# Performance work log

Hardware: AMD Instinct MI355X
Metric: run time of the kernel (lower is better)

## Reference

```python
import jax, jax.numpy as jnp
import numpy as np

NEG_SLOPE = 0.2  # PyG GATConv default negative_slope
H, C = 4, 64     # heads, per-head channels


def gat_layer(x, src, dst, edge_attr, W, a_src, a_dst, We, a_e, b):
    """PyG-style GATConv with edge features, concat=True. src/dst include self loops."""
    N = x.shape[0]
    h = (x @ W).reshape(N, H, C)                      # [N,H,C]
    al_s = (h * a_src[None]).sum(-1)                  # [N,H]
    al_d = (h * a_dst[None]).sum(-1)                  # [N,H]
    eh = (edge_attr @ We).reshape(-1, H, C)           # [E,H,C]
    al_e = (eh * a_e[None]).sum(-1)                   # [E,H]
    alpha = jax.nn.leaky_relu(al_s[src] + al_d[dst] + al_e, NEG_SLOPE)  # [E,H]
    # softmax over incoming edges of each destination node
    m = jax.ops.segment_max(alpha, dst, num_segments=N)
    p = jnp.exp(alpha - m[dst])
    denom = jax.ops.segment_sum(p, dst, num_segments=N)
    w = p / (denom[dst] + 1e-16)                      # [E,H]
    msg = h[src] * w[..., None]                       # [E,H,C]
    out = jax.ops.segment_sum(msg, dst, num_segments=N)  # [N,H,C]
    return out.reshape(N, H * C) + b


def setup_inputs() -> dict:
    key = jax.random.key(0)
    ks = jax.random.split(key, 20)
    N, E = 50000, 800000
    s = 0.05
    inp = {
        'x': jax.random.normal(ks[0], (N, 5), jnp.float32),
        'edge_index': jax.random.randint(ks[1], (2, E), 0, N, jnp.int32),
        'edge_attr': jax.random.normal(ks[2], (E, 4), jnp.float32),
        'W0': jax.random.normal(ks[3], (5, 256), jnp.float32) * s,
        'a_src0': jax.random.normal(ks[4], (H, C), jnp.float32) * s,
        'a_dst0': jax.random.normal(ks[5], (H, C), jnp.float32) * s,
        'We0': jax.random.normal(ks[6], (4, 256), jnp.float32) * s,
        'a_e0': jax.random.normal(ks[7], (H, C), jnp.float32) * s,
        'b0': jnp.zeros((256,), jnp.float32),
        'W1': jax.random.normal(ks[8], (256, 256), jnp.float32) * s,
        'a_src1': jax.random.normal(ks[9], (H, C), jnp.float32) * s,
        'a_dst1': jax.random.normal(ks[10], (H, C), jnp.float32) * s,
        'We1': jax.random.normal(ks[11], (4, 256), jnp.float32) * s,
        'a_e1': jax.random.normal(ks[12], (H, C), jnp.float32) * s,
        'b1': jnp.zeros((256,), jnp.float32),
        'Wm1': jax.random.normal(ks[13], (768, 128), jnp.float32) * s,
        'bm1': jnp.zeros((128,), jnp.float32),
        'Wm2': jax.random.normal(ks[14], (128, 64), jnp.float32) * s,
        'bm2': jnp.zeros((64,), jnp.float32),
        'Wm3': jax.random.normal(ks[15], (64, 128), jnp.float32) * s,
        'bm3': jnp.zeros((128,), jnp.float32),
    }
    return inp


def reference(x, edge_index, edge_attr,
              W0, a_src0, a_dst0, We0, a_e0, b0,
              W1, a_src1, a_dst1, We1, a_e1, b1,
              Wm1, bm1, Wm2, bm2, Wm3, bm3):
    N = x.shape[0]
    # add self loops once; self-loop edge_attr = mean of edge_attr (PyG fill_value='mean')
    loops = jnp.arange(N, dtype=edge_index.dtype)
    src = jnp.concatenate([edge_index[0], loops])
    dst = jnp.concatenate([edge_index[1], loops])
    mean_ea = jnp.mean(edge_attr, axis=0, keepdims=True)
    ea = jnp.concatenate([edge_attr, jnp.broadcast_to(mean_ea, (N, edge_attr.shape[1]))], axis=0)

    h = gat_layer(x, src, dst, ea, W0, a_src0, a_dst0, We0, a_e0, b0)
    h = jax.nn.relu(h)  # dropout is identity in eval
    h = gat_layer(h, src, dst, ea, W1, a_src1, a_dst1, We1, a_e1, b1)

    mean_pool = jnp.mean(h, axis=0)                      # [256]
    max_pool = jnp.max(h, axis=0)                        # [256]
    att = jax.nn.softmax(jnp.sum(h * mean_pool[None], axis=1))  # [N]
    att_pool = jnp.sum(h * att[:, None], axis=0)         # [256]
    comb = jnp.concatenate([mean_pool, max_pool, att_pool])  # [768]

    z = jax.nn.relu(comb @ Wm1 + bm1)
    z = jax.nn.relu(z @ Wm2 + bm2)
    g = z @ Wm3 + bm3
    return g[None]  # [1,128]
```

## Files before the change

### kernel.cpp

```cpp
#include <hip/hip_runtime.h>
#include <hip/hip_fp16.h>
#include <type_traits>

static const long long N_ = 50000;
static const long long E_ = 800000;
#define LOG2E 1.44269504088896f

typedef __attribute__((ext_vector_type(8))) short bf16x8;
typedef __attribute__((ext_vector_type(4))) float f32x4;

__device__ __forceinline__ float lrelu(float x){ return x >= 0.f ? x : 0.2f*x; }
__device__ __forceinline__ unsigned fkey(float x){
  unsigned u = __float_as_uint(x);
  return (u & 0x80000000u) ? ~u : (u | 0x80000000u);
}
__device__ __forceinline__ float unfkey(unsigned k){
  return __uint_as_float((k & 0x80000000u) ? (k & 0x7fffffffu) : ~k);
}
__device__ __forceinline__ unsigned h2u(__half2 h){ return *(unsigned*)&h; }

__global__ void k_pre(const int* __restrict__ ei, int* __restrict__ deg,
                      const float* __restrict__ ea, float* __restrict__ sum_ea,
                      const float* __restrict__ W1, ushort* __restrict__ Bhi,
                      ushort* __restrict__ Blo){
  int t = threadIdx.x;
  long long e = (long long)blockIdx.x*256 + t;
  if (e < E_) atomicAdd(&deg[ei[E_ + e]], 1);
  if (blockIdx.x < 256){
    int k = blockIdx.x, n = t;
    float v = W1[k*256+n];
    unsigned u = __float_as_uint(v);
    ushort hi = (ushort)(u>>16);
    float rem = v - __uint_as_float(u & 0xffff0000u);
    unsigned ur = __float_as_uint(rem);
    ushort lo = (ushort)((ur + 0x7fff + ((ur>>16)&1)) >> 16);
    int tl = n>>4, kb = k>>5, q = (k>>3)&3, j = k&7;
    long long idx = ((((long long)tl*8+kb)*64 + q*16 + (n&15))<<3) + j;
    Bhi[idx] = hi; Blo[idx] = lo;
  }
  __shared__ float lds[256];
  float s = 0.f;
  for (long long i = (long long)blockIdx.x*256 + t; i < E_*4; i += (long long)gridDim.x*256)
    s += ea[i];
  lds[t] = s; __syncthreads();
  for (int st=128; st>=4; st>>=1){ if (t<st) lds[t] += lds[t+st]; __syncthreads(); }
  if (t<4) atomicAdd(&sum_ea[t], lds[t]);
}

__global__ void k_scan1(const int* __restrict__ deg, int* __restrict__ bsum){
  __shared__ int lds[256];
  int t = threadIdx.x;
  long long idx = (long long)blockIdx.x*256 + t;
  lds[t] = (idx < N_) ? deg[idx] : 0;
  __syncthreads();
  for (int st=128; st>=1; st>>=1){ if (t<st) lds[t] += lds[t+st]; __syncthreads(); }
  if (t==0) bsum[blockIdx.x] = lds[0];
}

__global__ void k_scan2(const int* __restrict__ bsum, int* __restrict__ bpre, int nb,
                        int* __restrict__ rowptr,
                        const float* __restrict__ We0, const float* __restrict__ ae0,
                        const float* __restrict__ We1, const float* __restrict__ ae1,
                        const float* __restrict__ sum_ea, float* __restrict__ small){
  __shared__ int lds[256];
  int t = threadIdx.x;
  int v = (t < nb) ? bsum[t] : 0;
  lds[t] = v; __syncthreads();
  for (int off=1; off<256; off<<=1){
    int add = (t>=off) ? lds[t-off] : 0;
    __syncthreads();
    lds[t] += add;
    __syncthreads();
  }
  if (t < nb) bpre[t] = lds[t] - v;
  if (t == 0) rowptr[N_] = (int)E_;
  if (t < 32){
    int l = t>>4, f = (t>>2)&3, h = t&3;
    const float* We = l ? We1 : We0;
    const float* ae = l ? ae1 : ae0;
    float s = 0.f;
    for (int cc=0; cc<64; cc++) s += We[f*256 + h*64 + cc]*ae[h*64+cc];
    small[l*16 + f*4 + h] = s * LOG2E;
  }
  __syncthreads();
  if (t < 8){
    int l = t>>2, h = t&3;
    const float* Ae = small + l*16;
    const float invE = 1.f/(float)E_;
    float s = 0.f;
    for (int f=0; f<4; f++) s += sum_ea[f]*invE*Ae[f*4+h];
    small[32 + l*4 + h] = s;
  }
}

__global__ void k_scan3(const int* __restrict__ deg, const int* __restrict__ bpre,
                        int* __restrict__ rowptr, int* __restrict__ cursor){
  __shared__ int lds[256];
  int t = threadIdx.x;
  long long idx = (long long)blockIdx.x*256 + t;
  int v = (idx < N_) ? deg[idx] : 0;
  lds[t] = v; __syncthreads();
  for (int off=1; off<256; off<<=1){
    int add = (t>=off) ? lds[t-off] : 0;
    __syncthreads();
    lds[t] += add;
    __syncthreads();
  }
  if (idx < N_){
    int rp = bpre[blockIdx.x] + lds[t] - v;
    rowptr[idx] = rp; cursor[idx] = rp;
  }
}

__global__ void k_scatter(const int* __restrict__ ei, const float* __restrict__ ea,
                          int* __restrict__ cursor, int* __restrict__ csr_src,
                          __half* __restrict__ aleh, const float* __restrict__ small){
  long long e = (long long)blockIdx.x*256 + threadIdx.x;
  if (e >= E_) return;
  int s = ei[e], d = ei[E_+e];
  int pos = atomicAdd(&cursor[d], 1);
  csr_src[pos] = s;
  float4 v = *(const float4*)(ea + e*4);
  float o0[4], o1[4];
  #pragma unroll
  for (int h=0; h<4; h++){
    o0[h] = v.x*small[0+h]  + v.y*small[4+h]  + v.z*small[8+h]  + v.w*small[12+h];
    o1[h] = v.x*small[16+h] + v.y*small[20+h] + v.z*small[24+h] + v.w*small[28+h];
  }
  uint4 pk = make_uint4(h2u(__floats2half2_rn(o0[0],o0[1])),
                        h2u(__floats2half2_rn(o0[2],o0[3])),
                        h2u(__floats2half2_rn(o1[0],o1[1])),
                        h2u(__floats2half2_rn(o1[2],o1[3])));
  *(uint4*)(aleh + (long long)pos*8) = pk;
}

__global__ void k_h0(const float* __restrict__ x, const float* __restrict__ W0,
                     const float* __restrict__ as0, const float* __restrict__ ad0,
                     __half* __restrict__ h0, float* __restrict__ als, float* __restrict__ ald){
  int wid = (int)(((long long)blockIdx.x*blockDim.x + threadIdx.x) >> 6);
  int lane = threadIdx.x & 63;
  if (wid >= (int)N_) return;
  const float* xr = x + wid*5;
  float xv[5];
  #pragma unroll
  for (int f=0; f<5; f++) xv[f] = xr[f];
  int c = lane*4;
  float a0=0,a1=0,a2=0,a3=0;
  #pragma unroll
  for (int f=0; f<5; f++){
    const float* wr = W0 + f*256 + c;
    a0 += xv[f]*wr[0]; a1 += xv[f]*wr[1]; a2 += xv[f]*wr[2]; a3 += xv[f]*wr[3];
  }
  __half2 p01 = __floats2half2_rn(a0,a1);
  __half2 p23 = __floats2half2_rn(a2,a3);
  uint2 pk = make_uint2(h2u(p01), h2u(p23));
  *(uint2*)(h0 + wid*256 + c) = pk;
  const float* asp = as0 + c;
  const float* adp = ad0 + c;
  float ss = a0*asp[0]+a1*asp[1]+a2*asp[2]+a3*asp[3];
  float dd = a0*adp[0]+a1*adp[1]+a2*adp[2]+a3*adp[3];
  int head = lane>>4;
  #pragma unroll
  for (int m=1; m<16; m<<=1){ ss += __shfl_xor(ss, m); dd += __shfl_xor(dd, m); }
  if ((lane&15)==0){ als[wid*4+head]=ss*LOG2E; ald[wid*4+head]=dd*LOG2E; }
}

template<typename OutT, bool RELU>
__global__ __launch_bounds__(256) void k_agg(const __half* __restrict__ hin,
    const float* __restrict__ als, const float* __restrict__ ald,
    const int* __restrict__ rowptr, const int* __restrict__ csr_src,
    const __half* __restrict__ aleh,
    const float* __restrict__ small, int loop_off,
    const float* __restrict__ bias, OutT* __restrict__ out){
  int wid = (int)(((long long)blockIdx.x*256 + threadIdx.x) >> 6);
  int lane = threadIdx.x & 63;
  if (wid >= (int)N_) return;
  int head = lane>>4, c = lane*4;
  const uint2* hp = (const uint2*)hin;
  float aldv = ald[wid*4+head];
  float aS = lrelu(als[wid*4+head] + aldv + small[loop_off+head]);
  float mA = aS, dA = 1.f;
  uint2 pk0 = hp[wid*64 + lane];
  float2 f01 = __half22float2(*(__half2*)&pk0.x);
  float2 f23 = __half22float2(*(__half2*)&pk0.y);
  float aAx=f01.x, aAy=f01.y, aAz=f23.x, aAw=f23.y;
  float mB=-1e30f, dB=0.f, aBx=0.f, aBy=0.f, aBz=0.f, aBw=0.f;
  int beg = rowptr[wid], end = rowptr[wid+1];
  int i = beg;
  for (; i+3 < end; i+=4){
    int s0=csr_src[i], s1=csr_src[i+1], s2=csr_src[i+2], s3=csr_src[i+3];
    float t0=als[s0*4+head], t1=als[s1*4+head];
    float t2=als[s2*4+head], t3=als[s3*4+head];
    float e0=__half2float(aleh[i*8+head]);
    float e1=__half2float(aleh[(i+1)*8+head]);
    float e2=__half2float(aleh[(i+2)*8+head]);
    float e3=__half2float(aleh[(i+3)*8+head]);
    uint2 r0=hp[s0*64+lane], r1=hp[s1*64+lane];
    uint2 r2=hp[s2*64+lane], r3=hp[s3*64+lane];
    float a0=lrelu(t0+aldv+e0), a1=lrelu(t1+aldv+e1);
    float a2=lrelu(t2+aldv+e2), a3=lrelu(t3+aldv+e3);
    {
      float nm = fmaxf(mA, fmaxf(a0,a1));
      float sc = exp2f(mA-nm), p0 = exp2f(a0-nm), p1 = exp2f(a1-nm);
      float2 u01=__half22float2(*(__half2*)&r0.x), u23=__half22float2(*(__half2*)&r0.y);
      float2 v01=__half22float2(*(__half2*)&r1.x), v23=__half22float2(*(__half2*)&r1.y);
      dA  = dA*sc + p0 + p1;
      aAx = aAx*sc + p0*u01.x + p1*v01.x;
      aAy = aAy*sc + p0*u01.y + p1*v01.y;
      aAz = aAz*sc + p0*u23.x + p1*v23.x;
      aAw = aAw*sc + p0*u23.y + p1*v23.y;
      mA = nm;
    }
    {
      float nm = fmaxf(mB, fmaxf(a2,a3));
      float sc = exp2f(mB-nm), p2 = exp2f(a2-nm), p3 = exp2f(a3-nm);
      float2 u01=__half22float2(*(__half2*)&r2.x), u23=__half22float2(*(__half2*)&r2.y);
      float2 v01=__half22float2(*(__half2*)&r3.x), v23=__half22float2(*(__half2*)&r3.y);
      dB  = dB*sc + p2 + p3;
      aBx = aBx*sc + p2*u01.x + p3*v01.x;
      aBy = aBy*sc + p2*u01.y + p3*v01.y;
      aBz = aBz*sc + p2*u23.x + p3*v23.x;
      aBw = aBw*sc + p2*u23.y + p3*v23.y;
      mB = nm;
    }
  }
  for (; i < end; i++){
    int s0 = csr_src[i];
    float e0 = __half2float(aleh[i*8+head]);
    float a = lrelu(als[s0*4+head] + aldv + e0);
    uint2 r = hp[s0*64+lane];
    float nm = fmaxf(mA, a);
    float sc = exp2f(mA-nm), p = exp2f(a-nm);
    float2 g01=__half22float2(*(__half2*)&r.x), g23=__half22float2(*(__half2*)&r.y);
    dA  = dA*sc + p;
    aAx = aAx*sc + p*g01.x;
    aAy = aAy*sc + p*g01.y;
    aAz = aAz*sc + p*g23.x;
    aAw = aAw*sc + p*g23.y;
    mA = nm;
  }
  float nm = fmaxf(mA, mB);
  float sA = exp2f(mA-nm), sB = exp2f(mB-nm);
  float d  = dA*sA + dB*sB;
  float ax = aAx*sA + aBx*sB, ay = aAy*sA + aBy*sB;
  float az = aAz*sA + aBz*sB, aw = aAw*sA + aBw*sB;
  float inv = 1.f/(d + 1e-16f);
  const float* bp = bias + c;
  float ox = ax*inv + bp[0], oy = ay*inv + bp[1];
  float oz = az*inv + bp[2], ow = aw*inv + bp[3];
  if (RELU){ ox=fmaxf(ox,0.f); oy=fmaxf(oy,0.f); oz=fmaxf(oz,0.f); ow=fmaxf(ow,0.f); }
  if constexpr (std::is_same<OutT,__half>::value){
    uint2 qk = make_uint2(h2u(__floats2half2_rn(ox,oy)), h2u(__floats2half2_rn(oz,ow)));
    *(uint2*)(out + wid*256 + c) = qk;
  } else {
    *(float4*)(out + wid*256 + c) = make_float4(ox,oy,oz,ow);
  }
}

__global__ __launch_bounds__(256) void k_gemm(const float* __restrict__ A,
    const ushort* __restrict__ Bhi, const ushort* __restrict__ Blo,
    __half* __restrict__ Ch, const float* __restrict__ as1, const float* __restrict__ ad1,
    float* __restrict__ als, float* __restrict__ ald){
  __shared__ ushort Ah[32*264];
  __shared__ ushort Al[32*264];
  int t = threadIdx.x;
  long long base = (long long)blockIdx.x*32;
  for (int i=t; i<2048; i+=256){
    int r = i>>6, q4 = i&63;
    float4 v = make_float4(0.f,0.f,0.f,0.f);
    if (base + r < N_) v = *(const float4*)(A + (base+r)*256 + q4*4);
    float vv[4] = {v.x,v.y,v.z,v.w};
    ushort hh[4], ll[4];
    #pragma unroll
    for (int e=0;e<4;e++){
      unsigned u = __float_as_uint(vv[e]);
      hh[e] = (ushort)(u>>16);
      float rem = vv[e] - __uint_as_float(u & 0xffff0000u);
      unsigned ur = __float_as_uint(rem);
      ll[e] = (ushort)((ur + 0x7fff + ((ur>>16)&1)) >> 16);
    }
    int off = r*264 + q4*4;
    *(ushort4*)(Ah+off) = make_ushort4(hh[0],hh[1],hh[2],hh[3]);
    *(ushort4*)(Al+off) = make_ushort4(ll[0],ll[1],ll[2],ll[3]);
  }
  __syncthreads();
  int w = t>>6, lane = t&63, m = lane&15, q = lane>>4;
  int rbase = (w>>1)*16;
  int nhalf = (w&1)*8;
  f32x4 acc[8];
  #pragma unroll
  for (int i=0;i<8;i++) acc[i] = (f32x4){0.f,0.f,0.f,0.f};
  for (int kb=0; kb<8; kb++){
    int aoff = (rbase+m)*264 + kb*32 + q*8;
    bf16x8 ah = *(const bf16x8*)(Ah + aoff);
    bf16x8 al = *(const bf16x8*)(Al + aoff);
    #pragma unroll
    for (int tt=0; tt<8; tt++){
      long long bidx = ((((long long)(nhalf+tt)*8+kb)*64 + lane)<<3);
      bf16x8 bh = *(const bf16x8*)(Bhi + bidx);
      bf16x8 bl = *(const bf16x8*)(Blo + bidx);
      acc[tt] = __builtin_amdgcn_mfma_f32_16x16x32_bf16(ah, bh, acc[tt], 0,0,0);
      acc[tt] = __builtin_amdgcn_mfma_f32_16x16x32_bf16(al, bh, acc[tt], 0,0,0);
      acc[tt] = __builtin_amdgcn_mfma_f32_16x16x32_bf16(ah, bl, acc[tt], 0,0,0);
    }
  }
  float ssv[4][2], ddv[4][2];
  #pragma unroll
  for (int r=0;r<4;r++){ ssv[r][0]=0.f; ssv[r][1]=0.f; ddv[r][0]=0.f; ddv[r][1]=0.f; }
  #pragma unroll
  for (int tt=0; tt<8; tt++){
    int col = (nhalf+tt)*16 + m;
    float as_ = as1[col], ad_ = ad1[col];
    int hh = tt>>2;
    #pragma unroll
    for (int r=0;r<4;r++){
      ssv[r][hh] += acc[tt][r]*as_;
      ddv[r][hh] += acc[tt][r]*ad_;
    }
  }
  #pragma unroll
  for (int r=0;r<4;r++){
    #pragma unroll
    for (int hh=0; hh<2; hh++){
      #pragma unroll
      for (int mm=1; mm<16; mm<<=1){
        ssv[r][hh] += __shfl_xor(ssv[r][hh], mm);
        ddv[r][hh] += __shfl_xor(ddv[r][hh], mm);
      }
    }
  }
  #pragma unroll
  for (int r=0;r<4;r++){
    long long grow = base + rbase + q*4 + r;
    if (grow < N_){
      #pragma unroll
      for (int tt=0; tt<8; tt++)
        Ch[grow*256 + (nhalf+tt)*16 + m] = __float2half(acc[tt][r]);
      if (m==0){
        int hb = (w&1)*2;
        als[grow*4 + hb+0] = ssv[r][0]*LOG2E;
        ald[grow*4 + hb+0] = ddv[r][0]*LOG2E;
        als[grow*4 + hb+1] = ssv[r][1]*LOG2E;
        ald[grow*4 + hb+1] = ddv[r][1]*LOG2E;
      }
    }
  }
}

__global__ void k_pool1(const __half* __restrict__ h2, float* __restrict__ sum_pool,
                        unsigned* __restrict__ maxkey){
  int c = threadIdx.x;
  float s = 0.f; float m = -3.4e38f;
  for (long long n = blockIdx.x; n < N_; n += gridDim.x){
    float v = __half2float(h2[n*256+c]); s += v; m = fmaxf(m, v);
  }
  atomicAdd(&sum_pool[c], s);
  atomicMax(&maxkey[c], fkey(m));
}

__global__ void k_atts(const __half* __restrict__ h2, const float* __restrict__ sum_pool,
                       float* __restrict__ sarr, unsigned* __restrict__ smax){
  __shared__ float lmax[4];
  int t = threadIdx.x; int lane = t&63; int w = t>>6;
  const float invN = 1.f/(float)N_;
  int c = lane*4;
  float4 mp = *(const float4*)(sum_pool + c);
  float mymax = -3.4e38f;
  for (long long wid = (long long)blockIdx.x*4 + w; wid < N_; wid += (long long)gridDim.x*4){
    uint2 pk = *(const uint2*)(h2 + wid*256 + c);
    float2 a01 = __half22float2(*(__half2*)&pk.x);
    float2 a23 = __half22float2(*(__half2*)&pk.y);
    float s = (a01.x*mp.x + a01.y*mp.y + a23.x*mp.z + a23.y*mp.w)*invN;
    #pragma unroll
    for (int m=1; m<64; m<<=1) s += __shfl_xor(s, m);
    if (lane==0) sarr[wid] = s;
    mymax = fmaxf(mymax, s);
  }
  if (lane==0) lmax[w] = mymax;
  __syncthreads();
  if (t==0){
    float mm = fmaxf(fmaxf(lmax[0],lmax[1]), fmaxf(lmax[2],lmax[3]));
    atomicMax(smax, fkey(mm));
  }
}

__global__ void k_attd(const float* __restrict__ sarr, const unsigned* __restrict__ smax,
                       float* __restrict__ ssum){
  __shared__ float lds[256];
  int t = threadIdx.x;
  float mx = unfkey(*smax);
  float s = 0.f;
  for (long long i = (long long)blockIdx.x*256 + t; i < N_; i += (long long)gridDim.x*256)
    s += __expf(sarr[i] - mx);
  lds[t] = s; __syncthreads();
  for (int st=128; st>=1; st>>=1){ if (t<st) lds[t]+=lds[t+st]; __syncthreads(); }
  if (t==0) atomicAdd(ssum, lds[0]);
}

__global__ void k_attp(const __half* __restrict__ h2, const float* __restrict__ sarr,
                       const unsigned* __restrict__ smax, const float* __restrict__ ssum,
                       float* __restrict__ att_pool){
  int c = threadIdx.x;
  float mx = unfkey(*smax);
  float inv = 1.f/(*ssum);
  float acc = 0.f;
  for (long long n = blockIdx.x; n < N_; n += gridDim.x){
    float w = __expf(sarr[n]-mx)*inv;
    acc += __half2float(h2[n*256+c])*w;
  }
  atomicAdd(&att_pool[c], acc);
}

__global__ void k_mlp(const float* __restrict__ sum_pool, const unsigned* __restrict__ maxkey,
                      const float* __restrict__ att_pool,
                      const float* __restrict__ Wm1, const float* __restrict__ bm1,
                      const float* __restrict__ Wm2, const float* __restrict__ bm2,
                      const float* __restrict__ Wm3, const float* __restrict__ bm3,
                      float* __restrict__ out){
  __shared__ float comb[768];
  __shared__ float z1p[4][128]; __shared__ float z1[128];
  __shared__ float z2p[8][64];  __shared__ float z2[64];
  __shared__ float z3p[4][128];
  int t = threadIdx.x;
  const float invN = 1.f/(float)N_;
  for (int i=t; i<768; i+=512){
    float v;
    if (i < 256)      v = sum_pool[i]*invN;
    else if (i < 512) v = unfkey(maxkey[i-256]);
    else              v = att_pool[i-512];
    comb[i] = v;
  }
  __syncthreads();
  { int n = t&127, part = t>>7;
    float a = 0.f;
    for (int f=part*192; f<part*192+192; f++) a += comb[f]*Wm1[f*128+n];
    z1p[part][n] = a;
  }
  __syncthreads();
  if (t < 128)
    z1[t] = fmaxf(bm1[t] + z1p[0][t]+z1p[1][t]+z1p[2][t]+z1p[3][t], 0.f);
  __syncthreads();
  { int n = t&63, part = t>>6;
    float a = 0.f;
    for (int f=part*16; f<part*16+16; f++) a += z1[f]*Wm2[f*64+n];
    z2p[part][n] = a;
  }
  __syncthreads();
  if (t < 64){
    float a = bm2[t];
    #pragma unroll
    for (int p=0;p<8;p++) a += z2p[p][t];
    z2[t] = fmaxf(a, 0.f);
  }
  __syncthreads();
  { int n = t&127, part = t>>7;
    float a = 0.f;
    for (int f=part*16; f<part*16+16; f++) a += z2[f]*Wm3[f*128+n];
    z3p[part][n] = a;
  }
  __syncthreads();
  if (t < 128)
    out[t] = bm3[t] + z3p[0][t]+z3p[1][t]+z3p[2][t]+z3p[3][t];
}

extern "C" void kernel_launch(void* const* d_in, const int* in_sizes, int n_in,
                              void* d_out, int out_size, void* d_ws, size_t ws_size,
                              hipStream_t stream){
  (void)in_sizes; (void)n_in; (void)out_size; (void)ws_size;
  const float* x   = (const float*)d_in[0];
  const int*   ei  = (const int*)d_in[1];
  const float* ea  = (const float*)d_in[2];
  const float* W0  = (const float*)d_in[3];
  const float* as0 = (const float*)d_in[4];
  const float* ad0 = (const float*)d_in[5];
  const float* We0 = (const float*)d_in[6];
  const float* ae0 = (const float*)d_in[7];
  const float* b0  = (const float*)d_in[8];
  const float* W1  = (const float*)d_in[9];
  const float* as1 = (const float*)d_in[10];
  const float* ad1 = (const float*)d_in[11];
  const float* We1 = (const float*)d_in[12];
  const float* ae1 = (const float*)d_in[13];
  const float* b1  = (const float*)d_in[14];
  const float* Wm1 = (const float*)d_in[15];
  const float* bm1 = (const float*)d_in[16];
  const float* Wm2 = (const float*)d_in[17];
  const float* bm2 = (const float*)d_in[18];
  const float* Wm3 = (const float*)d_in[19];
  const float* bm3 = (const float*)d_in[20];
  float* out = (float*)d_out;

  char* ws = (char*)d_ws;
  size_t o = 0;
  auto alloc = [&](size_t bytes)->size_t{
    size_t r = o; o = (o + bytes + 255) & ~(size_t)255; return r;
  };
  size_t o_bufF   = alloc((size_t)N_*256*4);
  size_t o_bufH   = alloc((size_t)N_*256*2);
  size_t o_als0   = alloc((size_t)N_*4*4);
  size_t o_ald0   = alloc((size_t)N_*4*4);
  size_t o_als1   = alloc((size_t)N_*4*4);
  size_t o_ald1   = alloc((size_t)N_*4*4);
  size_t o_rowptr = alloc((size_t)(N_+1)*4);
  size_t o_cursor = alloc((size_t)N_*4);
  size_t o_csrsrc = alloc((size_t)E_*4);
  size_t o_ale    = alloc((size_t)E_*8*2);
  size_t o_sarr   = alloc((size_t)N_*4);
  size_t o_Bhi    = alloc((size_t)256*256*2);
  size_t o_Blo    = alloc((size_t)256*256*2);
  size_t o_bsum   = alloc(256*4);
  size_t o_bpre   = alloc(256*4);
  size_t zstart   = o;
  size_t o_deg    = alloc((size_t)N_*4);
  size_t o_sumea  = alloc(16);
  size_t o_sumpool= alloc(256*4);
  size_t o_maxkey = alloc(256*4);
  size_t o_attpool= alloc(256*4);
  size_t o_smax   = alloc(4);
  size_t o_ssum   = alloc(4);
  size_t zend     = o;
  size_t o_small  = alloc(40*4);

  float*  bufF   = (float*)(ws + o_bufF);
  __half* bufH   = (__half*)(ws + o_bufH);
  __half* h2h    = (__half*)(ws + o_bufF);
  float* pals0  = (float*)(ws + o_als0);
  float* pald0  = (float*)(ws + o_ald0);
  float* pals1  = (float*)(ws + o_als1);
  float* pald1  = (float*)(ws + o_ald1);
  int*   rowptr = (int*)(ws + o_rowptr);
  int*   cursor = (int*)(ws + o_cursor);
  int*   csrsrc = (int*)(ws + o_csrsrc);
  __half* aleh  = (__half*)(ws + o_ale);
  float* sarr   = (float*)(ws + o_sarr);
  ushort* Bhi   = (ushort*)(ws + o_Bhi);
  ushort* Blo   = (ushort*)(ws + o_Blo);
  int*   bsum   = (int*)(ws + o_bsum);
  int*   bpre   = (int*)(ws + o_bpre);
  int*   deg    = (int*)(ws + o_deg);
  float* sumea  = (float*)(ws + o_sumea);
  float* sumpool= (float*)(ws + o_sumpool);
  unsigned* maxkey = (unsigned*)(ws + o_maxkey);
  float* attpool= (float*)(ws + o_attpool);
  unsigned* smax= (unsigned*)(ws + o_smax);
  float* ssum   = (float*)(ws + o_ssum);
  float* small  = (float*)(ws + o_small);

  hipMemsetAsync(ws + zstart, 0, zend - zstart, stream);

  int eb = (int)((E_ + 255)/256);
  int nb_wave = (int)((N_*64 + 255)/256);
  int gb = (int)((N_ + 31)/32);
  int sb = (int)((N_ + 255)/256);

  k_pre    <<<eb, 256, 0, stream>>>(ei, deg, ea, sumea, W1, Bhi, Blo);
  k_scan1  <<<sb, 256, 0, stream>>>(deg, bsum);
  k_scan2  <<<1, 256, 0, stream>>>(bsum, bpre, sb, rowptr,
                                   We0, ae0, We1, ae1, sumea, small);
  k_scan3  <<<sb, 256, 0, stream>>>(deg, bpre, rowptr, cursor);
  k_scatter<<<eb, 256, 0, stream>>>(ei, ea, cursor, csrsrc, aleh, small);
  k_h0     <<<nb_wave, 256, 0, stream>>>(x, W0, as0, ad0, bufH, pals0, pald0);
  k_agg<float,true>  <<<nb_wave, 256, 0, stream>>>(bufH, pals0, pald0, rowptr, csrsrc,
                                         aleh + 0, small, 32, b0, bufF);
  k_gemm   <<<gb, 256, 0, stream>>>(bufF, Bhi, Blo, bufH, as1, ad1, pals1, pald1);
  k_agg<__half,false><<<nb_wave, 256, 0, stream>>>(bufH, pals1, pald1, rowptr, csrsrc,
                                         aleh + 4, small, 36, b1, h2h);
  k_pool1  <<<256, 256, 0, stream>>>(h2h, sumpool, maxkey);
  k_atts   <<<1024, 256, 0, stream>>>(h2h, sumpool, sarr, smax);
  k_attd   <<<128, 256, 0, stream>>>(sarr, smax, ssum);
  k_attp   <<<256, 256, 0, stream>>>(h2h, sarr, smax, ssum, attpool);
  k_mlp    <<<1, 512, 0, stream>>>(sumpool, maxkey, attpool,
                                   Wm1, bm1, Wm2, bm2, Wm3, bm3, out);
}
```

Measured before the change: 562.9 us.

## Precompute unnormalized edge softmax weights and drop max-subtraction in aggregation and attention pooling

Edge attention exponentials are now computed per edge up front: during the CSR scatter for layer 0, and in a new per-edge kernel for layer 1. Both are stored as fp16, so the aggregation kernel becomes a plain weighted sum without online-softmax rescaling, and its unroll goes up to 8 gathers. The attention-pooling softmax also skips max subtraction, which removes one kernel and an atomic max. This relies on logits staying small enough not to overflow exp or fp16. It adds an extra edge pass and a csr_dst array.

```diff
diff --git a/kernel.cpp b/kernel.cpp
--- a/kernel.cpp
+++ b/kernel.cpp
@@ -112,28 +112,6 @@
   }
 }
 
-__global__ void k_scatter(const int* __restrict__ ei, const float* __restrict__ ea,
-                          int* __restrict__ cursor, int* __restrict__ csr_src,
-                          __half* __restrict__ aleh, const float* __restrict__ small){
-  long long e = (long long)blockIdx.x*256 + threadIdx.x;
-  if (e >= E_) return;
-  int s = ei[e], d = ei[E_+e];
-  int pos = atomicAdd(&cursor[d], 1);
-  csr_src[pos] = s;
-  float4 v = *(const float4*)(ea + e*4);
-  float o0[4], o1[4];
-  #pragma unroll
-  for (int h=0; h<4; h++){
-    o0[h] = v.x*small[0+h]  + v.y*small[4+h]  + v.z*small[8+h]  + v.w*small[12+h];
-    o1[h] = v.x*small[16+h] + v.y*small[20+h] + v.z*small[24+h] + v.w*small[28+h];
-  }
-  uint4 pk = make_uint4(h2u(__floats2half2_rn(o0[0],o0[1])),
-                        h2u(__floats2half2_rn(o0[2],o0[3])),
-                        h2u(__floats2half2_rn(o1[0],o1[1])),
-                        h2u(__floats2half2_rn(o1[2],o1[3])));
-  *(uint4*)(aleh + (long long)pos*8) = pk;
-}
-
 __global__ void k_h0(const float* __restrict__ x, const float* __restrict__ W0,
                      const float* __restrict__ as0, const float* __restrict__ ad0,
                      __half* __restrict__ h0, float* __restrict__ als, float* __restrict__ ald){
@@ -151,9 +129,7 @@
     const float* wr = W0 + f*256 + c;
     a0 += xv[f]*wr[0]; a1 += xv[f]*wr[1]; a2 += xv[f]*wr[2]; a3 += xv[f]*wr[3];
   }
-  __half2 p01 = __floats2half2_rn(a0,a1);
-  __half2 p23 = __floats2half2_rn(a2,a3);
-  uint2 pk = make_uint2(h2u(p01), h2u(p23));
+  uint2 pk = make_uint2(h2u(__floats2half2_rn(a0,a1)), h2u(__floats2half2_rn(a2,a3)));
   *(uint2*)(h0 + wid*256 + c) = pk;
   const float* asp = as0 + c;
   const float* adp = ad0 + c;
@@ -165,11 +141,61 @@
   if ((lane&15)==0){ als[wid*4+head]=ss*LOG2E; ald[wid*4+head]=dd*LOG2E; }
 }
 
+__global__ void k_scatter(const int* __restrict__ ei, const float* __restrict__ ea,
+                          int* __restrict__ cursor, int* __restrict__ csr_src,
+                          int* __restrict__ csr_dst,
+                          __half* __restrict__ ale1h, __half* __restrict__ p0h,
+                          const float* __restrict__ small,
+                          const float* __restrict__ als0, const float* __restrict__ ald0){
+  long long e = (long long)blockIdx.x*256 + threadIdx.x;
+  if (e >= E_) return;
+  int s = ei[e], d = ei[E_+e];
+  int pos = atomicAdd(&cursor[d], 1);
+  csr_src[pos] = s;
+  csr_dst[pos] = d;
+  float4 v = *(const float4*)(ea + e*4);
+  float4 As = *(const float4*)(als0 + s*4);
+  float4 Ad = *(const float4*)(ald0 + d*4);
+  float as_[4] = {As.x,As.y,As.z,As.w};
+  float ad_[4] = {Ad.x,Ad.y,Ad.z,Ad.w};
+  float p0[4], o1[4];
+  #pragma unroll
+  for (int h=0; h<4; h++){
+    float a0 = v.x*small[0+h]  + v.y*small[4+h]  + v.z*small[8+h]  + v.w*small[12+h];
+    p0[h] = exp2f(lrelu(as_[h] + ad_[h] + a0));
+    o1[h] = v.x*small[16+h] + v.y*small[20+h] + v.z*small[24+h] + v.w*small[28+h];
+  }
+  uint2 pkp = make_uint2(h2u(__floats2half2_rn(p0[0],p0[1])), h2u(__floats2half2_rn(p0[2],p0[3])));
+  uint2 pke = make_uint2(h2u(__floats2half2_rn(o1[0],o1[1])), h2u(__floats2half2_rn(o1[2],o1[3])));
+  *(uint2*)(p0h + (long long)pos*4) = pkp;
+  *(uint2*)(ale1h + (long long)pos*4) = pke;
+}
+
+__global__ void k_palpha1(const int* __restrict__ csr_src, const int* __restrict__ csr_dst,
+                          const __half* __restrict__ ale1h,
+                          const float* __restrict__ als1, const float* __restrict__ ald1,
+                          __half* __restrict__ p1h){
+  long long i = (long long)blockIdx.x*256 + threadIdx.x;
+  if (i >= E_) return;
+  int s = csr_src[i], d = csr_dst[i];
+  float4 As = *(const float4*)(als1 + s*4);
+  float4 Ad = *(const float4*)(ald1 + d*4);
+  uint2 pke = *(const uint2*)(ale1h + i*4);
+  float2 e01 = __half22float2(*(__half2*)&pke.x);
+  float2 e23 = __half22float2(*(__half2*)&pke.y);
+  float p0 = exp2f(lrelu(As.x+Ad.x+e01.x));
+  float p1 = exp2f(lrelu(As.y+Ad.y+e01.y));
+  float p2 = exp2f(lrelu(As.z+Ad.z+e23.x));
+  float p3 = exp2f(lrelu(As.w+Ad.w+e23.y));
+  uint2 pk = make_uint2(h2u(__floats2half2_rn(p0,p1)), h2u(__floats2half2_rn(p2,p3)));
+  *(uint2*)(p1h + i*4) = pk;
+}
+
 template<typename OutT, bool RELU>
 __global__ __launch_bounds__(256) void k_agg(const __half* __restrict__ hin,
     const float* __restrict__ als, const float* __restrict__ ald,
     const int* __restrict__ rowptr, const int* __restrict__ csr_src,
-    const __half* __restrict__ aleh,
+    const __half* __restrict__ ph,
     const float* __restrict__ small, int loop_off,
     const float* __restrict__ bias, OutT* __restrict__ out){
   int wid = (int)(((long long)blockIdx.x*256 + threadIdx.x) >> 6);
@@ -177,74 +203,42 @@
   if (wid >= (int)N_) return;
   int head = lane>>4, c = lane*4;
   const uint2* hp = (const uint2*)hin;
-  float aldv = ald[wid*4+head];
-  float aS = lrelu(als[wid*4+head] + aldv + small[loop_off+head]);
-  float mA = aS, dA = 1.f;
-  uint2 pk0 = hp[wid*64 + lane];
-  float2 f01 = __half22float2(*(__half2*)&pk0.x);
-  float2 f23 = __half22float2(*(__half2*)&pk0.y);
-  float aAx=f01.x, aAy=f01.y, aAz=f23.x, aAw=f23.y;
-  float mB=-1e30f, dB=0.f, aBx=0.f, aBy=0.f, aBz=0.f, aBw=0.f;
+  float aS = lrelu(als[wid*4+head] + ald[wid*4+head] + small[loop_off+head]);
+  float pS = exp2f(aS);
+  uint2 r0 = hp[wid*64 + lane];
+  float2 f01 = __half22float2(*(__half2*)&r0.x);
+  float2 f23 = __half22float2(*(__half2*)&r0.y);
+  float den = pS;
+  float ax = pS*f01.x, ay = pS*f01.y, az = pS*f23.x, aw = pS*f23.y;
   int beg = rowptr[wid], end = rowptr[wid+1];
   int i = beg;
-  for (; i+3 < end; i+=4){
-    int s0=csr_src[i], s1=csr_src[i+1], s2=csr_src[i+2], s3=csr_src[i+3];
-    float t0=als[s0*4+head], t1=als[s1*4+head];
-    float t2=als[s2*4+head], t3=als[s3*4+head];
-    float e0=__half2float(aleh[i*8+head]);
-    float e1=__half2float(aleh[(i+1)*8+head]);
-    float e2=__half2float(aleh[(i+2)*8+head]);
-    float e3=__half2float(aleh[(i+3)*8+head]);
-    uint2 r0=hp[s0*64+lane], r1=hp[s1*64+lane];
-    uint2 r2=hp[s2*64+lane], r3=hp[s3*64+lane];
-    float a0=lrelu(t0+aldv+e0), a1=lrelu(t1+aldv+e1);
-    float a2=lrelu(t2+aldv+e2), a3=lrelu(t3+aldv+e3);
-    {
-      float nm = fmaxf(mA, fmaxf(a0,a1));
-      float sc = exp2f(mA-nm), p0 = exp2f(a0-nm), p1 = exp2f(a1-nm);
-      float2 u01=__half22float2(*(__half2*)&r0.x), u23=__half22float2(*(__half2*)&r0.y);
-      float2 v01=__half22float2(*(__half2*)&r1.x), v23=__half22float2(*(__half2*)&r1.y);
-      dA  = dA*sc + p0 + p1;
-      aAx = aAx*sc + p0*u01.x + p1*v01.x;
-      aAy = aAy*sc + p0*u01.y + p1*v01.y;
-      aAz = aAz*sc + p0*u23.x + p1*v23.x;
-      aAw = aAw*sc + p0*u23.y + p1*v23.y;
-      mA = nm;
-    }
-    {
-      float nm = fmaxf(mB, fmaxf(a2,a3));
-      float sc = exp2f(mB-nm), p2 = exp2f(a2-nm), p3 = exp2f(a3-nm);
-      float2 u01=__half22float2(*(__half2*)&r2.x), u23=__half22float2(*(__half2*)&r2.y);
-      float2 v01=__half22float2(*(__half2*)&r3.x), v23=__half22float2(*(__half2*)&r3.y);
-      dB  = dB*sc + p2 + p3;
-      aBx = aBx*sc + p2*u01.x + p3*v01.x;
-      aBy = aBy*sc + p2*u01.y + p3*v01.y;
-      aBz = aBz*sc + p2*u23.x + p3*v23.x;
-      aBw = aBw*sc + p2*u23.y + p3*v23.y;
-      mB = nm;
+  for (; i+7 < end; i += 8){
+    int   sidx[8]; float pv[8]; uint2 rr[8];
+    #pragma unroll
+    for (int k=0;k<8;k++) sidx[k] = csr_src[i+k];
+    #pragma unroll
+    for (int k=0;k<8;k++) pv[k] = __half2float(ph[(i+k)*4+head]);
+    #pragma unroll
+    for (int k=0;k<8;k++) rr[k] = hp[sidx[k]*64+lane];
+    #pragma unroll
+    for (int k=0;k<8;k++){
+      float2 u01 = __half22float2(*(__half2*)&rr[k].x);
+      float2 u23 = __half22float2(*(__half2*)&rr[k].y);
+      den += pv[k];
+      ax += pv[k]*u01.x; ay += pv[k]*u01.y;
+      az += pv[k]*u23.x; aw += pv[k]*u23.y;
     }
   }
   for (; i < end; i++){
     int s0 = csr_src[i];
-    float e0 = __half2float(aleh[i*8+head]);
-    float a = lrelu(als[s0*4+head] + aldv + e0);
+    float p = __half2float(ph[i*4+head]);
     uint2 r = hp[s0*64+lane];
-    float nm = fmaxf(mA, a);
-    float sc = exp2f(mA-nm), p = exp2f(a-nm);
-    float2 g01=__half22float2(*(__half2*)&r.x), g23=__half22float2(*(__half2*)&r.y);
-    dA  = dA*sc + p;
-    aAx = aAx*sc + p*g01.x;
-    aAy = aAy*sc + p*g01.y;
-    aAz = aAz*sc + p*g23.x;
-    aAw = aAw*sc + p*g23.y;
-    mA = nm;
-  }
-  float nm = fmaxf(mA, mB);
-  float sA = exp2f(mA-nm), sB = exp2f(mB-nm);
-  float d  = dA*sA + dB*sB;
-  float ax = aAx*sA + aBx*sB, ay = aAy*sA + aBy*sB;
-  float az = aAz*sA + aBz*sB, aw = aAw*sA + aBw*sB;
-  float inv = 1.f/(d + 1e-16f);
+    float2 u01 = __half22float2(*(__half2*)&r.x);
+    float2 u23 = __half22float2(*(__half2*)&r.y);
+    den += p;
+    ax += p*u01.x; ay += p*u01.y; az += p*u23.x; aw += p*u23.y;
+  }
+  float inv = 1.f/(den + 1e-16f);
   const float* bp = bias + c;
   float ox = ax*inv + bp[0], oy = ay*inv + bp[1];
   float oz = az*inv + bp[2], ow = aw*inv + bp[3];
@@ -359,13 +353,13 @@
 }
 
 __global__ void k_atts(const __half* __restrict__ h2, const float* __restrict__ sum_pool,
-                       float* __restrict__ sarr, unsigned* __restrict__ smax){
-  __shared__ float lmax[4];
+                       float* __restrict__ sarr, float* __restrict__ ssum){
+  __shared__ float lsum[4];
   int t = threadIdx.x; int lane = t&63; int w = t>>6;
   const float invN = 1.f/(float)N_;
   int c = lane*4;
   float4 mp = *(const float4*)(sum_pool + c);
-  float mymax = -3.4e38f;
+  float esum = 0.f;
   for (long long wid = (long long)blockIdx.x*4 + w; wid < N_; wid += (long long)gridDim.x*4){
     uint2 pk = *(const uint2*)(h2 + wid*256 + c);
     float2 a01 = __half22float2(*(__half2*)&pk.x);
@@ -373,39 +367,20 @@
     float s = (a01.x*mp.x + a01.y*mp.y + a23.x*mp.z + a23.y*mp.w)*invN;
     #pragma unroll
     for (int m=1; m<64; m<<=1) s += __shfl_xor(s, m);
-    if (lane==0) sarr[wid] = s;
-    mymax = fmaxf(mymax, s);
-  }
-  if (lane==0) lmax[w] = mymax;
-  __syncthreads();
-  if (t==0){
-    float mm = fmaxf(fmaxf(lmax[0],lmax[1]), fmaxf(lmax[2],lmax[3]));
-    atomicMax(smax, fkey(mm));
-  }
-}
-
-__global__ void k_attd(const float* __restrict__ sarr, const unsigned* __restrict__ smax,
-                       float* __restrict__ ssum){
-  __shared__ float lds[256];
-  int t = threadIdx.x;
-  float mx = unfkey(*smax);
-  float s = 0.f;
-  for (long long i = (long long)blockIdx.x*256 + t; i < N_; i += (long long)gridDim.x*256)
-    s += __expf(sarr[i] - mx);
-  lds[t] = s; __syncthreads();
-  for (int st=128; st>=1; st>>=1){ if (t<st) lds[t]+=lds[t+st]; __syncthreads(); }
-  if (t==0) atomicAdd(ssum, lds[0]);
+    if (lane==0){ sarr[wid] = s; esum += __expf(s); }
+  }
+  if (lane==0) lsum[w] = esum;
+  __syncthreads();
+  if (t==0) atomicAdd(ssum, lsum[0]+lsum[1]+lsum[2]+lsum[3]);
 }
 
 __global__ void k_attp(const __half* __restrict__ h2, const float* __restrict__ sarr,
-                       const unsigned* __restrict__ smax, const float* __restrict__ ssum,
-                       float* __restrict__ att_pool){
+                       const float* __restrict__ ssum, float* __restrict__ att_pool){
   int c = threadIdx.x;
-  float mx = unfkey(*smax);
   float inv = 1.f/(*ssum);
   float acc = 0.f;
   for (long long n = blockIdx.x; n < N_; n += gridDim.x){
-    float w = __expf(sarr[n]-mx)*inv;
+    float w = __expf(sarr[n])*inv;
     acc += __half2float(h2[n*256+c])*w;
   }
   atomicAdd(&att_pool[c], acc);
@@ -504,7 +479,10 @@
   size_t o_rowptr = alloc((size_t)(N_+1)*4);
   size_t o_cursor = alloc((size_t)N_*4);
   size_t o_csrsrc = alloc((size_t)E_*4);
-  size_t o_ale    = alloc((size_t)E_*8*2);
+  size_t o_csrdst = alloc((size_t)E_*4);
+  size_t o_ale1   = alloc((size_t)E_*4*2);
+  size_t o_p0     = alloc((size_t)E_*4*2);
+  size_t o_p1     = alloc((size_t)E_*4*2);
   size_t o_sarr   = alloc((size_t)N_*4);
   size_t o_Bhi    = alloc((size_t)256*256*2);
   size_t o_Blo    = alloc((size_t)256*256*2);
@@ -516,7 +494,6 @@
   size_t o_sumpool= alloc(256*4);
   size_t o_maxkey = alloc(256*4);
   size_t o_attpool= alloc(256*4);
-  size_t o_smax   = alloc(4);
   size_t o_ssum   = alloc(4);
   size_t zend     = o;
   size_t o_small  = alloc(40*4);
@@ -531,7 +508,10 @@
   int*   rowptr = (int*)(ws + o_rowptr);
   int*   cursor = (int*)(ws + o_cursor);
   int*   csrsrc = (int*)(ws + o_csrsrc);
-  __half* aleh  = (__half*)(ws + o_ale);
+  int*   csrdst = (int*)(ws + o_csrdst);
+  __half* ale1h = (__half*)(ws + o_ale1);
+  __half* p0h   = (__half*)(ws + o_p0);
+  __half* p1h   = (__half*)(ws + o_p1);
   float* sarr   = (float*)(ws + o_sarr);
   ushort* Bhi   = (ushort*)(ws + o_Bhi);
   ushort* Blo   = (ushort*)(ws + o_Blo);
@@ -542,7 +522,6 @@
   float* sumpool= (float*)(ws + o_sumpool);
   unsigned* maxkey = (unsigned*)(ws + o_maxkey);
   float* attpool= (float*)(ws + o_attpool);
-  unsigned* smax= (unsigned*)(ws + o_smax);
   float* ssum   = (float*)(ws + o_ssum);
   float* small  = (float*)(ws + o_small);
 
@@ -558,17 +537,18 @@
   k_scan2  <<<1, 256, 0, stream>>>(bsum, bpre, sb, rowptr,
                                    We0, ae0, We1, ae1, sumea, small);
   k_scan3  <<<sb, 256, 0, stream>>>(deg, bpre, rowptr, cursor);
-  k_scatter<<<eb, 256, 0, stream>>>(ei, ea, cursor, csrsrc, aleh, small);
   k_h0     <<<nb_wave, 256, 0, stream>>>(x, W0, as0, ad0, bufH, pals0, pald0);
+  k_scatter<<<eb, 256, 0, stream>>>(ei, ea, cursor, csrsrc, csrdst,
+                                    ale1h, p0h, small, pals0, pald0);
   k_agg<float,true>  <<<nb_wave, 256, 0, stream>>>(bufH, pals0, pald0, rowptr, csrsrc,
-                                         aleh + 0, small, 32, b0, bufF);
+                                         p0h, small, 32, b0, bufF);
   k_gemm   <<<gb, 256, 0, stream>>>(bufF, Bhi, Blo, bufH, as1, ad1, pals1, pald1);
+  k_palpha1<<<eb, 256, 0, stream>>>(csrsrc, csrdst, ale1h, pals1, pald1, p1h);
   k_agg<__half,false><<<nb_wave, 256, 0, stream>>>(bufH, pals1, pald1, rowptr, csrsrc,
-                                         aleh + 4, small, 36, b1, h2h);
+                                         p1h, small, 36, b1, h2h);
   k_pool1  <<<256, 256, 0, stream>>>(h2h, sumpool, maxkey);
-  k_atts   <<<1024, 256, 0, stream>>>(h2h, sumpool, sarr, smax);
-  k_attd   <<<128, 256, 0, stream>>>(sarr, smax, ssum);
-  k_attp   <<<256, 256, 0, stream>>>(h2h, sarr, smax, ssum, attpool);
+  k_atts   <<<1024, 256, 0, stream>>>(h2h, sumpool, sarr, ssum);
+  k_attp   <<<256, 256, 0, stream>>>(h2h, sarr, ssum, attpool);
   k_mlp    <<<1, 512, 0, stream>>>(sumpool, maxkey, attpool,
                                    Wm1, bm1, Wm2, bm2, Wm3, bm3, out);
 }
```

New measurement: 569.3 us. No clear change (+1.1%).
